# Performance work log

Measured on AMD Instinct MI355X. Metric: run time of the kernel, lower is better.

The kernel has to match this reference:

```python
import jax, jax.numpy as jnp
import numpy as np

MODEL_DIM = 1024
NUM_HEADS = 16
HEAD_DIM = MODEL_DIM // NUM_HEADS
BATCH = 16
KEY_LEN = 4096


def setup_inputs() -> dict:
    key = jax.random.key(0)
    ks = jax.random.split(key, 10)
    u = lambda k, shape: jax.random.uniform(k, shape, jnp.float32, -0.5, 0.5)
    return {
        "hidden_states": jax.random.normal(ks[0], (BATCH, 1, MODEL_DIM), jnp.float32),
        "key_value_states": jax.random.normal(ks[1], (BATCH, KEY_LEN, MODEL_DIM), jnp.float32),
        "Wq": u(ks[2], (MODEL_DIM, MODEL_DIM)), "bq": u(ks[3], (MODEL_DIM,)),
        "Wk": u(ks[4], (MODEL_DIM, MODEL_DIM)), "bk": u(ks[5], (MODEL_DIM,)),
        "Wv": u(ks[6], (MODEL_DIM, MODEL_DIM)), "bv": u(ks[7], (MODEL_DIM,)),
        "Wo": u(ks[8], (MODEL_DIM, MODEL_DIM)), "bo": u(ks[9], (MODEL_DIM,)),
    }


def reference(hidden_states, key_value_states, Wq, bq, Wk, bk, Wv, bv, Wo, bo):
    B, K = key_value_states.shape[0], key_value_states.shape[1]
    H, Dh = NUM_HEADS, HEAD_DIM
    # projections (nn.Linear: x @ W.T + b)
    q = hidden_states @ Wq.T + bq            # [B, 1, H*Dh]
    k = key_value_states @ Wk.T + bk         # [B, K, H*Dh]
    v = key_value_states @ Wv.T + bv         # [B, K, H*Dh]
    # split heads
    q = q.reshape(B, 1, H, Dh).transpose(0, 2, 1, 3)   # [B, H, 1, Dh]
    k = k.reshape(B, K, H, Dh).transpose(0, 2, 1, 3)   # [B, H, K, Dh]
    v = v.reshape(B, K, H, Dh).transpose(0, 2, 1, 3)   # [B, H, K, Dh]
    q = q / jnp.sqrt(jnp.asarray(Dh, q.dtype))
    # scores: [B, H, K] (query_len == 1, squeezed)
    scores = jnp.einsum("bhqd,bhkd->bhqk", q, k)[:, :, 0, :]
    # Hardtanh(min_val=0, max_val=1) gate instead of softmax; dropout p=0
    attn = jnp.clip(scores, 0.0, 1.0)                  # [B, H, K]
    # broadcast-multiply with value, merge heads back
    context = attn[..., None] * v                      # [B, H, K, Dh]
    context = context.transpose(0, 2, 1, 3).reshape(B, K, H * Dh)
    output = context @ Wo.T + bo                       # [B, K, model_dim]
    return output
```

## Files before the change

### kernel.cpp

```cpp
#include <hip/hip_runtime.h>
#include <hip/hip_bf16.h>
#include <stdint.h>

typedef __bf16 bf16x8 __attribute__((ext_vector_type(8)));
typedef __bf16 bf16x4 __attribute__((ext_vector_type(4)));
typedef float  f32x4  __attribute__((ext_vector_type(4)));

#define B_  16
#define KL  4096
#define D_  1024
#define NH  16
#define NROWS (B_*KL)

__device__ __forceinline__ void gload_lds16(const void* g, void* l) {
  __builtin_amdgcn_global_load_lds(
      (__attribute__((address_space(1))) void*)g,
      (__attribute__((address_space(3))) void*)l, 16, 0, 0);
}


__global__ __launch_bounds__(256) void conv_bf16_kernel(const float* __restrict__ s,
                                                        __bf16* __restrict__ d, int n4) {
  int i = blockIdx.x * 256 + threadIdx.x;
  if (i >= n4) return;
  float4 v = reinterpret_cast<const float4*>(s)[i];
  bf16x4 o;
  o[0] = (__bf16)v.x; o[1] = (__bf16)v.y; o[2] = (__bf16)v.z; o[3] = (__bf16)v.w;
  *reinterpret_cast<bf16x4*>(d + (size_t)i * 4) = o;
}

__global__ __launch_bounds__(256) void qproj_kernel(const float* __restrict__ hs,
                                                    const float* __restrict__ Wq,
                                                    const float* __restrict__ bq,
                                                    float* __restrict__ q) {
  int gid = blockIdx.x * 256 + threadIdx.x;
  int b = gid >> 10, j = gid & 1023;
  const float* x = hs + (size_t)b * D_;
  const float* w = Wq + (size_t)j * D_;
  float acc = 0.f;
  for (int i = 0; i < D_; i += 4) {
    float4 xv = *reinterpret_cast<const float4*>(x + i);
    float4 wv = *reinterpret_cast<const float4*>(w + i);
    acc += xv.x*wv.x + xv.y*wv.y + xv.z*wv.z + xv.w*wv.w;
  }
  q[gid] = (acc + bq[j]) * 0.125f;
}

__global__ __launch_bounds__(256) void wqeff_kernel(const float* __restrict__ q,
                                                    const float* __restrict__ Wk,
                                                    const float* __restrict__ bk,
                                                    __bf16* __restrict__ whi,
                                                    __bf16* __restrict__ wlo,
                                                    float* __restrict__ cb) {
  const int h = blockIdx.x, b = blockIdx.y;
  const int tid = threadIdx.x;
  __shared__ float ql[64];
  if (tid < 64) ql[tid] = q[(size_t)b * D_ + h * 64 + tid];
  __syncthreads();
  float a0 = 0, a1 = 0, a2 = 0, a3 = 0;
  for (int d = 0; d < 64; ++d) {
    float qv = ql[d];
    const float* wr = Wk + (size_t)(h * 64 + d) * D_;
    a0 += qv * wr[tid];
    a1 += qv * wr[tid + 256];
    a2 += qv * wr[tid + 512];
    a3 += qv * wr[tid + 768];
  }
  const size_t base = ((size_t)b * NH + h) * D_;
  float a[4] = {a0, a1, a2, a3};
#pragma unroll
  for (int j = 0; j < 4; ++j) {
    __bf16 hi = (__bf16)a[j];
    whi[base + j * 256 + tid] = hi;
    wlo[base + j * 256 + tid] = (__bf16)(a[j] - (float)hi);
  }
  if (tid < 64) {
    float p = ql[tid] * bk[h * 64 + tid];
    p += __shfl_down(p, 32); p += __shfl_down(p, 16); p += __shfl_down(p, 8);
    p += __shfl_down(p, 4);  p += __shfl_down(p, 2);  p += __shfl_down(p, 1);
    if (tid == 0) cb[b * NH + h] = p;
  }
}

__global__ __launch_bounds__(256) void scores_mfma_kernel(
    const float* __restrict__ kvs,
    const __bf16* __restrict__ whi,
    const __bf16* __restrict__ wlo,
    const float* __restrict__ cb,
    float* __restrict__ attn,
    __bf16* __restrict__ kvd) {
  const int b = blockIdx.y;
  const int tid = threadIdx.x;
  const int lane = tid & 63, wv = tid >> 6;
  const int r16 = lane & 15, kgrp = lane >> 4;
  const int row0 = blockIdx.x * 64 + wv * 16;
  const size_t grow = (size_t)b * KL + row0;

  const float* xrow = kvs + (grow + r16) * D_ + kgrp * 8;
  __bf16*      krow = kvd + (grow + r16) * D_ + kgrp * 8;
  const __bf16* wh = whi + ((size_t)b * NH + r16) * D_ + kgrp * 8;
  const __bf16* wl = wlo + ((size_t)b * NH + r16) * D_ + kgrp * 8;

  f32x4 acc = {};
  for (int k0 = 0; k0 < D_; k0 += 32) {
    float4 x0 = *reinterpret_cast<const float4*>(xrow + k0);
    float4 x1 = *reinterpret_cast<const float4*>(xrow + k0 + 4);
    float xs[8] = {x0.x, x0.y, x0.z, x0.w, x1.x, x1.y, x1.z, x1.w};
    bf16x8 hi, lo;
#pragma unroll
    for (int i = 0; i < 8; ++i) {
      __bf16 h = (__bf16)xs[i];
      hi[i] = h;
      lo[i] = (__bf16)(xs[i] - (float)h);
    }
    *reinterpret_cast<bf16x8*>(krow + k0) = hi;
    bf16x8 bh = *reinterpret_cast<const bf16x8*>(wh + k0);
    bf16x8 bl = *reinterpret_cast<const bf16x8*>(wl + k0);
    acc = __builtin_amdgcn_mfma_f32_16x16x32_bf16(hi, bh, acc, 0, 0, 0);
    acc = __builtin_amdgcn_mfma_f32_16x16x32_bf16(hi, bl, acc, 0, 0, 0);
    acc = __builtin_amdgcn_mfma_f32_16x16x32_bf16(lo, bh, acc, 0, 0, 0);
  }
  const float c = cb[b * NH + r16];
#pragma unroll
  for (int r = 0; r < 4; ++r) {
    const int orow = row0 + kgrp * 4 + r;
    float s = acc[r] + c;
    attn[((size_t)b * KL + orow) * NH + r16] = fminf(fmaxf(s, 0.f), 1.f);
  }
}

template <bool GATE>
__global__ __launch_bounds__(512, 2) void gemm_nt(const __bf16* __restrict__ A,
                                                  const __bf16* __restrict__ Bt,
                                                  const float* __restrict__ bias,
                                                  const float* __restrict__ gate,
                                                  void* __restrict__ Cp) {
  __shared__ __bf16 As[2][256 * 64];
  __shared__ __bf16 Bs[2][256 * 64];
  const int tid = threadIdx.x;
  const int lane = tid & 63, wid = tid >> 6;
  const int wm = wid >> 2, wn = wid & 3;
  const int r16 = lane & 15, kgrp = lane >> 4;
  const int bswz = (blockIdx.x & 7) * 128 + (blockIdx.x >> 3);
  const int m0 = (bswz >> 2) * 256;
  const int n0 = (bswz & 3) * 256;

  const int srow = lane >> 3;
  const int scol = ((lane & 7) ^ srow) * 8;

  const int sw0 = ((kgrp) ^ (r16 & 7)) * 8;
  const int sw1 = ((4 + kgrp) ^ (r16 & 7)) * 8;

  f32x4 acc[8][4] = {};

#define STAGE_HALF(dstbuf, srcp, base0, h, k0)                                  \
  {                                                                             \
    _Pragma("unroll") for (int j = 0; j < 2; ++j) {                             \
      const int c = (h) * 16 + wid * 2 + j;                                     \
      gload_lds16((srcp) + (size_t)((base0) + c * 8 + srow) * D_ + (k0) + scol, \
                  &(dstbuf)[c * 512]);                                          \
    }                                                                           \
  }

#define LOAD_BV(Bb, sw)                                                         \
  _Pragma("unroll") for (int nh = 0; nh < 2; ++nh)                              \
    _Pragma("unroll") for (int g = 0; g < 2; ++g)                               \
      bv[nh * 2 + g] = *reinterpret_cast<const bf16x8*>(                        \
          &(Bb)[(nh * 128 + wn * 32 + g * 16 + r16) * 64 + (sw)]);

#define LOAD_AV(Ab, mh, sw)                                                     \
  _Pragma("unroll") for (int f = 0; f < 4; ++f)                                 \
    av[f] = *reinterpret_cast<const bf16x8*>(                                   \
        &(Ab)[((mh) * 128 + wm * 64 + f * 16 + r16) * 64 + (sw)]);

#define MFMA_PHASE(mh)                                                          \
  {                                                                             \
    __builtin_amdgcn_s_setprio(1);                                              \
    _Pragma("unroll") for (int f = 0; f < 4; ++f)                               \
      _Pragma("unroll") for (int q = 0; q < 4; ++q)                             \
        acc[(mh) * 4 + f][q] = __builtin_amdgcn_mfma_f32_16x16x32_bf16(         \
            av[f], bv[q], acc[(mh) * 4 + f][q], 0, 0, 0);                       \
    __builtin_amdgcn_s_setprio(0);                                              \
  }

#define WAITLGKM()                                                              \
  asm volatile("s_waitcnt lgkmcnt(0)" ::: "memory");                            \
  __builtin_amdgcn_sched_barrier(0);

  STAGE_HALF(Bs[0], Bt, n0, 0, 0);
  STAGE_HALF(Bs[0], Bt, n0, 1, 0);
  STAGE_HALF(As[0], A,  m0, 0, 0);
  STAGE_HALF(As[0], A,  m0, 1, 0);
  asm volatile("s_waitcnt vmcnt(2)" ::: "memory");
  __builtin_amdgcn_s_barrier();

  const int NT = D_ / 64;
  for (int t = 0; t < NT; ++t) {
    __bf16* Ab = (t & 1) ? As[1] : As[0];
    __bf16* Bb = (t & 1) ? Bs[1] : Bs[0];
    __bf16* An = (t & 1) ? As[0] : As[1];
    __bf16* Bn = (t & 1) ? Bs[0] : Bs[1];
    const int k1 = (t + 1) * 64;
    const bool pf = (t < NT - 1);
    bf16x8 bv[4], av[4];

    LOAD_BV(Bb, sw0);
    LOAD_AV(Ab, 0, sw0);
    if (pf) {
      STAGE_HALF(Bn, Bt, n0, 0, k1);
      STAGE_HALF(Bn, Bt, n0, 1, k1);
      STAGE_HALF(An, A,  m0, 0, k1);
      STAGE_HALF(An, A,  m0, 1, k1);
    }
    __builtin_amdgcn_s_barrier();
    WAITLGKM();
    MFMA_PHASE(0);
    if (pf) asm volatile("s_waitcnt vmcnt(8)" ::: "memory");
    else    asm volatile("s_waitcnt vmcnt(0)" ::: "memory");
    __builtin_amdgcn_s_barrier();
    LOAD_AV(Ab, 1, sw0);
    __builtin_amdgcn_s_barrier();
    WAITLGKM();
    MFMA_PHASE(1);
    __builtin_amdgcn_s_barrier();
    LOAD_BV(Bb, sw1);
    LOAD_AV(Ab, 0, sw1);
    __builtin_amdgcn_s_barrier();
    WAITLGKM();
    MFMA_PHASE(0);
    __builtin_amdgcn_s_barrier();
    LOAD_AV(Ab, 1, sw1);
    __builtin_amdgcn_s_barrier();
    WAITLGKM();
    MFMA_PHASE(1);
    if (pf) asm volatile("s_waitcnt vmcnt(2)" ::: "memory");
    __builtin_amdgcn_s_barrier();
  }

#pragma unroll
  for (int mh = 0; mh < 2; ++mh) {
#pragma unroll
    for (int f = 0; f < 4; ++f) {
      const int row0 = m0 + mh * 128 + wm * 64 + f * 16 + kgrp * 4;
#pragma unroll
      for (int nh = 0; nh < 2; ++nh) {
#pragma unroll
        for (int g = 0; g < 2; ++g) {
          const int col = n0 + nh * 128 + wn * 32 + g * 16 + r16;
          const float bc = bias[col];
          const int head = col >> 6;
          f32x4 v = acc[mh * 4 + f][nh * 2 + g];
#pragma unroll
          for (int r = 0; r < 4; ++r) {
            const int row = row0 + r;
            if constexpr (GATE) {
              float gg = gate[(size_t)row * NH + head];
              ((__bf16*)Cp)[(size_t)row * D_ + col] = (__bf16)((v[r] + bc) * gg);
            } else {
              ((float*)Cp)[(size_t)row * D_ + col] = v[r] + bc;
            }
          }
        }
      }
    }
  }
#undef STAGE_HALF
#undef LOAD_BV
#undef LOAD_AV
#undef MFMA_PHASE
#undef WAITLGKM
}

extern "C" void kernel_launch(void* const* d_in, const int* in_sizes, int n_in,
                              void* d_out, int out_size, void* d_ws, size_t ws_size,
                              hipStream_t stream) {
  const float* hs  = (const float*)d_in[0];
  const float* kvs = (const float*)d_in[1];
  const float* Wq  = (const float*)d_in[2];
  const float* bq  = (const float*)d_in[3];
  const float* Wk  = (const float*)d_in[4];
  const float* bk  = (const float*)d_in[5];
  const float* Wv  = (const float*)d_in[6];
  const float* bv  = (const float*)d_in[7];
  const float* Wo  = (const float*)d_in[8];
  const float* bo  = (const float*)d_in[9];
  float* out = (float*)d_out;

  char* w = (char*)d_ws;
  __bf16* ctx  = (__bf16*)w;  w += (size_t)NROWS * D_ * 2;
  float*  attn = (float*)w;   w += (size_t)NROWS * NH * 4;
  __bf16* WvB  = (__bf16*)w;  w += (size_t)D_ * D_ * 2;
  __bf16* WoB  = (__bf16*)w;  w += (size_t)D_ * D_ * 2;
  __bf16* whi  = (__bf16*)w;  w += (size_t)B_ * NH * D_ * 2;
  __bf16* wlo  = (__bf16*)w;  w += (size_t)B_ * NH * D_ * 2;
  float*  qbuf = (float*)w;   w += (size_t)B_ * D_ * 4;
  float*  cbuf = (float*)w;   w += B_ * NH * 4;

  __bf16* kvsB = (__bf16*)d_out;

  conv_bf16_kernel<<<1024, 256, 0, stream>>>(Wv, WvB, 262144);
  conv_bf16_kernel<<<1024, 256, 0, stream>>>(Wo, WoB, 262144);
  qproj_kernel<<<64, 256, 0, stream>>>(hs, Wq, bq, qbuf);
  wqeff_kernel<<<dim3(NH, B_), 256, 0, stream>>>(qbuf, Wk, bk, whi, wlo, cbuf);
  scores_mfma_kernel<<<dim3(KL / 64, B_), 256, 0, stream>>>(kvs, whi, wlo, cbuf, attn, kvsB);
  gemm_nt<true ><<<1024, 512, 0, stream>>>(kvsB, WvB, bv, attn, ctx);
  gemm_nt<false><<<1024, 512, 0, stream>>>(ctx, WoB, bo, (const float*)nullptr, (void*)out);
}
```

Baseline: 509.0 us.

## Prefetch gate-kernel inputs and strip barriers from GEMM main loop

The score kernel now loads the next iteration's float inputs and the weight fragments before doing the current conversion. It also splits the three MFMAs across two accumulators to shorten the dependency chain. In the bf16 GEMM, most intra-iteration barriers and explicit lgkmcnt waits are removed, and one A-half stage is deferred until after the first MFMA phase, so LDS reads overlap MFMAs with less synchronisation. Removing the barriers and waits depends on compiler-inserted waits for correctness and could expose LDS races around the buffer that is being staged.

After: 537.9 us. 1.06x slower.

```diff
diff --git a/kernel.cpp b/kernel.cpp
--- a/kernel.cpp
+++ b/kernel.cpp
@@ -101,10 +101,17 @@
   const __bf16* wh = whi + ((size_t)b * NH + r16) * D_ + kgrp * 8;
   const __bf16* wl = wlo + ((size_t)b * NH + r16) * D_ + kgrp * 8;
 
-  f32x4 acc = {};
+  f32x4 acc0 = {}, acc1 = {};
+  float4 x0 = *reinterpret_cast<const float4*>(xrow);
+  float4 x1 = *reinterpret_cast<const float4*>(xrow + 4);
   for (int k0 = 0; k0 < D_; k0 += 32) {
-    float4 x0 = *reinterpret_cast<const float4*>(xrow + k0);
-    float4 x1 = *reinterpret_cast<const float4*>(xrow + k0 + 4);
+    float4 n0, n1;
+    if (k0 + 32 < D_) {
+      n0 = *reinterpret_cast<const float4*>(xrow + k0 + 32);
+      n1 = *reinterpret_cast<const float4*>(xrow + k0 + 36);
+    }
+    bf16x8 bh = *reinterpret_cast<const bf16x8*>(wh + k0);
+    bf16x8 bl = *reinterpret_cast<const bf16x8*>(wl + k0);
     float xs[8] = {x0.x, x0.y, x0.z, x0.w, x1.x, x1.y, x1.z, x1.w};
     bf16x8 hi, lo;
 #pragma unroll
@@ -114,17 +121,16 @@
       lo[i] = (__bf16)(xs[i] - (float)h);
     }
     *reinterpret_cast<bf16x8*>(krow + k0) = hi;
-    bf16x8 bh = *reinterpret_cast<const bf16x8*>(wh + k0);
-    bf16x8 bl = *reinterpret_cast<const bf16x8*>(wl + k0);
-    acc = __builtin_amdgcn_mfma_f32_16x16x32_bf16(hi, bh, acc, 0, 0, 0);
-    acc = __builtin_amdgcn_mfma_f32_16x16x32_bf16(hi, bl, acc, 0, 0, 0);
-    acc = __builtin_amdgcn_mfma_f32_16x16x32_bf16(lo, bh, acc, 0, 0, 0);
+    acc0 = __builtin_amdgcn_mfma_f32_16x16x32_bf16(hi, bh, acc0, 0, 0, 0);
+    acc1 = __builtin_amdgcn_mfma_f32_16x16x32_bf16(hi, bl, acc1, 0, 0, 0);
+    acc1 = __builtin_amdgcn_mfma_f32_16x16x32_bf16(lo, bh, acc1, 0, 0, 0);
+    x0 = n0; x1 = n1;
   }
   const float c = cb[b * NH + r16];
 #pragma unroll
   for (int r = 0; r < 4; ++r) {
     const int orow = row0 + kgrp * 4 + r;
-    float s = acc[r] + c;
+    float s = acc0[r] + acc1[r] + c;
     attn[((size_t)b * KL + orow) * NH + r16] = fminf(fmaxf(s, 0.f), 1.f);
   }
 }
@@ -183,10 +189,6 @@
     __builtin_amdgcn_s_setprio(0);                                              \
   }
 
-#define WAITLGKM()                                                              \
-  asm volatile("s_waitcnt lgkmcnt(0)" ::: "memory");                            \
-  __builtin_amdgcn_sched_barrier(0);
-
   STAGE_HALF(Bs[0], Bt, n0, 0, 0);
   STAGE_HALF(Bs[0], Bt, n0, 1, 0);
   STAGE_HALF(As[0], A,  m0, 0, 0);
@@ -204,37 +206,29 @@
     const bool pf = (t < NT - 1);
     bf16x8 bv[4], av[4];
 
-    LOAD_BV(Bb, sw0);
-    LOAD_AV(Ab, 0, sw0);
     if (pf) {
       STAGE_HALF(Bn, Bt, n0, 0, k1);
       STAGE_HALF(Bn, Bt, n0, 1, k1);
       STAGE_HALF(An, A,  m0, 0, k1);
-      STAGE_HALF(An, A,  m0, 1, k1);
-    }
-    __builtin_amdgcn_s_barrier();
-    WAITLGKM();
+    }
+    LOAD_BV(Bb, sw0);
+    LOAD_AV(Ab, 0, sw0);
     MFMA_PHASE(0);
-    if (pf) asm volatile("s_waitcnt vmcnt(8)" ::: "memory");
+    if (pf) asm volatile("s_waitcnt vmcnt(6)" ::: "memory");
     else    asm volatile("s_waitcnt vmcnt(0)" ::: "memory");
     __builtin_amdgcn_s_barrier();
+    if (pf) STAGE_HALF(An, A, m0, 1, k1);
     LOAD_AV(Ab, 1, sw0);
-    __builtin_amdgcn_s_barrier();
-    WAITLGKM();
     MFMA_PHASE(1);
-    __builtin_amdgcn_s_barrier();
     LOAD_BV(Bb, sw1);
     LOAD_AV(Ab, 0, sw1);
-    __builtin_amdgcn_s_barrier();
-    WAITLGKM();
     MFMA_PHASE(0);
-    __builtin_amdgcn_s_barrier();
     LOAD_AV(Ab, 1, sw1);
-    __builtin_amdgcn_s_barrier();
-    WAITLGKM();
     MFMA_PHASE(1);
-    if (pf) asm volatile("s_waitcnt vmcnt(2)" ::: "memory");
-    __builtin_amdgcn_s_barrier();
+    if (pf) {
+      asm volatile("s_waitcnt vmcnt(2)" ::: "memory");
+      __builtin_amdgcn_s_barrier();
+    }
   }
 
 #pragma unroll
@@ -268,7 +262,6 @@
 #undef LOAD_BV
 #undef LOAD_AV
 #undef MFMA_PHASE
-#undef WAITLGKM
 }
 
 extern "C" void kernel_launch(void* const* d_in, const int* in_sizes, int n_in,
```
